# Performance work log

Measured on AMD Instinct MI355X. Metric: run time of the kernel, lower is better.

## Reference

```python
import jax, jax.numpy as jnp
import numpy as np

HIDDEN = 4096
N_HEADS = 32
NOPE = 128
ROPE = 64
Q_HEAD = NOPE + ROPE  # 192
V_HEAD = 128
KV_RANK = 512
EPS = 1e-6
THETA = 10000.0
SEQ = 2048


def setup_inputs() -> dict:
    key = jax.random.key(0)
    ks = jax.random.split(key, 6)
    s = lambda fi, fo: (2.0 / (fi + fo)) ** 0.5
    return {
        "positions": jnp.arange(SEQ, dtype=jnp.int64),
        "hidden_states": jax.random.normal(ks[0], (SEQ, HIDDEN), dtype=jnp.float32),
        "Wq": jax.random.normal(ks[1], (HIDDEN, N_HEADS * Q_HEAD), dtype=jnp.float32) * s(HIDDEN, N_HEADS * Q_HEAD),
        "Wkv_a": jax.random.normal(ks[2], (HIDDEN, KV_RANK + ROPE), dtype=jnp.float32) * s(HIDDEN, KV_RANK + ROPE),
        "ln_w": jnp.ones((KV_RANK,), dtype=jnp.float32),
        "Wkv_b": jax.random.normal(ks[3], (KV_RANK, N_HEADS * (NOPE + V_HEAD)), dtype=jnp.float32) * s(KV_RANK, N_HEADS * (NOPE + V_HEAD)),
        "Wo": jax.random.normal(ks[4], (N_HEADS * V_HEAD, HIDDEN), dtype=jnp.float32) * s(N_HEADS * V_HEAD, HIDDEN),
    }


def _rms_norm(x, w, eps=EPS):
    xf = x.astype(jnp.float32)
    var = jnp.mean(xf * xf, axis=-1, keepdims=True)
    return w * (xf * jax.lax.rsqrt(var + eps)).astype(x.dtype)


def _rope_cos_sin(positions):
    # neox-style rotary over ROPE dims
    inv_freq = 1.0 / (THETA ** (jnp.arange(0, ROPE, 2, dtype=jnp.float32) / ROPE))  # [ROPE/2]
    ang = positions.astype(jnp.float32)[:, None] * inv_freq[None, :]  # [S, ROPE/2]
    return jnp.cos(ang), jnp.sin(ang)


def _apply_rope(x, cos, sin):
    # x: [..., S, ROPE]; rotate-half (neox) convention
    x1, x2 = x[..., : ROPE // 2], x[..., ROPE // 2 :]
    return jnp.concatenate([x1 * cos - x2 * sin, x2 * cos + x1 * sin], axis=-1)


def reference(positions, hidden_states, Wq, Wkv_a, ln_w, Wkv_b, Wo):
    S = hidden_states.shape[0]
    scaling = Q_HEAD ** (-0.5)

    q = (hidden_states @ Wq).reshape(S, N_HEADS, Q_HEAD)
    q_pass, q_rot = q[..., :NOPE], q[..., NOPE:]

    ckv = hidden_states @ Wkv_a  # [S, KV_RANK + ROPE]
    k_lora, k_rot = ckv[:, :KV_RANK], ckv[:, KV_RANK:]

    kv = (_rms_norm(k_lora, ln_w) @ Wkv_b).reshape(S, N_HEADS, NOPE + V_HEAD)
    k_pass, v = kv[..., :NOPE], kv[..., NOPE:]

    cos, sin = _rope_cos_sin(positions)
    q_rot = _apply_rope(q_rot, cos[:, None, :], sin[:, None, :])  # [S,H,ROPE]
    k_rot = _apply_rope(k_rot, cos, sin)  # [S,ROPE], shared across heads

    qs = jnp.concatenate([q_pass, q_rot], axis=-1)  # [S,H,192]
    ks = jnp.concatenate([k_pass, jnp.broadcast_to(k_rot[:, None, :], (S, N_HEADS, ROPE))], axis=-1)

    # causal SDPA (value padded to q_head_dim then sliced back, as in source)
    scores = jnp.einsum("shd,thd->hst", qs, ks) * scaling  # [H,S,S]
    mask = jnp.tril(jnp.ones((S, S), dtype=bool))
    scores = jnp.where(mask[None], scores, jnp.finfo(scores.dtype).min)
    probs = jax.nn.softmax(scores, axis=-1)
    out = jnp.einsum("hst,thd->shd", probs, v)  # [S,H,V_HEAD]

    return out.reshape(S, N_HEADS * V_HEAD) @ Wo
```

## Files before the change

kernel.cpp:

```cpp
#include <hip/hip_runtime.h>


typedef __bf16 bf16x8 __attribute__((ext_vector_type(8)));
typedef float f32x4 __attribute__((ext_vector_type(4)));

#define SEQLEN 2048
#define NH 32
#define QH 192
#define QCN 6912
#define KVN 8192
#define HID 4096

#define AS1 __attribute__((address_space(1)))
#define AS3 __attribute__((address_space(3)))

__device__ __forceinline__ unsigned short f2b(float f) {
  union { float f; unsigned int u; } x; x.f = f;
  unsigned int r = (x.u + 0x7FFFu + ((x.u >> 16) & 1u)) >> 16;
  return (unsigned short)r;
}
__device__ __forceinline__ float b2f(unsigned short b) {
  union { unsigned int u; float f; } x; x.u = ((unsigned int)b) << 16;
  return x.f;
}

__global__ __launch_bounds__(256) void convk(const float* __restrict__ in,
                                             unsigned short* __restrict__ out,
                                             int n4) {
  int i = blockIdx.x * 256 + threadIdx.x;
  if (i < n4) {
    float4 v = ((const float4*)in)[i];
    ushort4 o;
    o.x = f2b(v.x); o.y = f2b(v.y); o.z = f2b(v.z); o.w = f2b(v.w);
    ((ushort4*)out)[i] = o;
  }
}

__global__ __launch_bounds__(256) void tconv(const float* __restrict__ in,
                                             unsigned short* __restrict__ out,
                                             int R, int Cin, int Cp) {
  __shared__ float t[64][65];
  const int r0 = blockIdx.x * 64, c0 = blockIdx.y * 64;
  const int tid = threadIdx.x;
#pragma unroll
  for (int i = 0; i < 16; ++i) {
    int idx = tid + i * 256;
    int rr = idx >> 6, cc = idx & 63;
    int c = c0 + cc;
    t[rr][cc] = (c < Cin) ? in[(size_t)(r0 + rr) * Cin + c] : 0.f;
  }
  __syncthreads();
#pragma unroll
  for (int i = 0; i < 16; ++i) {
    int idx = tid + i * 256;
    int cc = idx >> 6, rr = idx & 63;
    out[(size_t)(c0 + cc) * R + (r0 + rr)] = f2b(t[rr][cc]);
  }
}

template <int MH, int MHALF, int PAIR>
__device__ __forceinline__ void mmaq(f32x4 (*acc)[4], const bf16x8* aR, const bf16x8* bX) {
  __builtin_amdgcn_s_setprio(1);
#pragma unroll
  for (int i2 = 0; i2 < MH; ++i2)
#pragma unroll
    for (int kk = 0; kk < 2; ++kk)
#pragma unroll
      for (int j = 0; j < 2; ++j)
        acc[MHALF * MH + i2][PAIR * 2 + j] = __builtin_amdgcn_mfma_f32_16x16x32_bf16(
            aR[i2 * 2 + kk], bX[j * 2 + kk], acc[MHALF * MH + i2][PAIR * 2 + j], 0, 0, 0);
  __builtin_amdgcn_s_setprio(0);
}

#define PH_SYNC()                                        \
  __builtin_amdgcn_s_barrier();                          \
  asm volatile("s_waitcnt lgkmcnt(0)" ::: "memory");     \
  __builtin_amdgcn_sched_barrier(0)
#define PH_END() __builtin_amdgcn_s_barrier()

template <int BM, typename OutT>
__global__ __launch_bounds__(512, 2) void gemm8p(const unsigned short* __restrict__ A,
                                                 const unsigned short* __restrict__ B,
                                                 OutT* __restrict__ C,
                                                 int M, int N, int K) {
  constexpr int MF = BM / 32;
  constexpr int MH = MF / 2;
  constexpr int ARND = BM / 128;
  __shared__ __align__(16) unsigned short As[2][2][BM * 32];
  __shared__ __align__(16) unsigned short Bs[2][2][8192];

  const int tid = threadIdx.x;
  const int lane = tid & 63;
  const int w = tid >> 6;
  const int wr = w >> 2, wc = w & 3;
  const int l15 = lane & 15, lg = lane >> 4;
  const int ntn = N >> 8;
  const int bm = blockIdx.x / ntn, bn = blockIdx.x % ntn;
  const int m0 = bm * BM, n0 = bn << 8;

  auto stA = [&](int t, int h) {
    const int buf = t & 1, k0 = t << 6;
#pragma unroll
    for (int r = 0; r < ARND; ++r) {
      int u = r * 512 + tid;
      int blk = u >> 6, l = u & 63;
      int row = (blk >> 1) * 16 + (l & 15);
      int col = (blk & 1) * 32 + ((l >> 4) << 3);
      __builtin_amdgcn_global_load_lds(
          (const AS1 void*)(A + (size_t)(m0 + h * (BM / 2) + row) * K + (k0 + col)),
          (AS3 void*)(&As[buf][h][u * 8]), 16, 0, 0);
    }
  };
  auto stB = [&](int t, int h) {
    const int buf = t & 1, k0 = t << 6;
#pragma unroll
    for (int r = 0; r < 2; ++r) {
      int u = r * 512 + tid;
      int blk = u >> 6, l = u & 63;
      int row = (blk >> 1) * 16 + (l & 15);
      int col = (blk & 1) * 32 + ((l >> 4) << 3);
      __builtin_amdgcn_global_load_lds(
          (const AS1 void*)(B + (size_t)(n0 + h * 128 + row) * K + (k0 + col)),
          (AS3 void*)(&Bs[buf][h][u * 8]), 16, 0, 0);
    }
  };

  const f32x4 zero4 = {0.f, 0.f, 0.f, 0.f};
  f32x4 acc[MF][4];
#pragma unroll
  for (int i = 0; i < MF; ++i)
#pragma unroll
    for (int j = 0; j < 4; ++j) acc[i][j] = zero4;

  bf16x8 aR[MF], bA[4], bB[4];
  auto ldA = [&](int buf, int mhalf) {
#pragma unroll
    for (int i2 = 0; i2 < MH; ++i2)
#pragma unroll
      for (int kk = 0; kk < 2; ++kk)
        aR[i2 * 2 + kk] =
            *(const bf16x8*)&As[buf][wr][(((mhalf * MH + i2) * 2 + kk) * 64 + lane) * 8];
  };
  auto ldB = [&](int buf, int pair, bf16x8* dst) {
#pragma unroll
    for (int j = 0; j < 2; ++j)
#pragma unroll
      for (int kk = 0; kk < 2; ++kk)
        dst[j * 2 + kk] = *(const bf16x8*)
            &Bs[buf][wc >> 1][((((wc & 1) * 4 + pair * 2 + j) * 2 + kk) * 64 + lane) * 8];
  };

  const int nk = K >> 6;
  const int ni = nk >> 1;

  stA(0, 0); stA(0, 1); stB(0, 0); stB(0, 1);
  stB(1, 0); stB(1, 1);
  asm volatile("s_waitcnt vmcnt(4)" ::: "memory");
  __builtin_amdgcn_s_barrier();

#pragma unroll 1
  for (int i = 0; i < ni; ++i) {
    const int tO = 2 * i + 1, tN = 2 * i + 2, tN1 = 2 * i + 3;
    const bool pfN = tN < nk, pfN1 = tN1 < nk;
    const bool steady = (i + 1 < ni);
    ldA(0, 0); ldB(0, 0, bA); stA(tO, 0);
    PH_SYNC(); mmaq<MH, 0, 0>(acc, aR, bA); PH_END();
    ldB(0, 1, bB); stA(tO, 1);
    PH_SYNC(); mmaq<MH, 0, 1>(acc, aR, bB); PH_END();
    ldA(0, 1); if (pfN) stB(tN, 0);
    PH_SYNC(); mmaq<MH, 1, 1>(acc, aR, bB); PH_END();
    if (pfN) stB(tN, 1);
    if (steady) { asm volatile("s_waitcnt vmcnt(4)" ::: "memory"); }
    else        { asm volatile("s_waitcnt vmcnt(0)" ::: "memory"); }
    PH_SYNC(); mmaq<MH, 1, 0>(acc, aR, bA); PH_END();
    ldA(1, 0); ldB(1, 0, bA); if (pfN) stA(tN, 0);
    PH_SYNC(); mmaq<MH, 0, 0>(acc, aR, bA); PH_END();
    ldB(1, 1, bB); if (pfN) stA(tN, 1);
    PH_SYNC(); mmaq<MH, 0, 1>(acc, aR, bB); PH_END();
    ldA(1, 1); if (pfN1) stB(tN1, 0);
    PH_SYNC(); mmaq<MH, 1, 1>(acc, aR, bB); PH_END();
    if (pfN1) stB(tN1, 1);
    if (steady) { asm volatile("s_waitcnt vmcnt(4)" ::: "memory"); }
    else        { asm volatile("s_waitcnt vmcnt(0)" ::: "memory"); }
    PH_SYNC(); mmaq<MH, 1, 0>(acc, aR, bA); PH_END();
  }

  const int r0 = m0 + wr * (BM / 2), c0 = n0 + wc * 64;
#pragma unroll
  for (int mf = 0; mf < MF; ++mf)
#pragma unroll
    for (int nf = 0; nf < 4; ++nf) {
      int r = r0 + mf * 16 + lg * 4;
      int c = c0 + nf * 16 + l15;
#pragma unroll
      for (int i = 0; i < 4; ++i) {
        float v = acc[mf][nf][i];
        if constexpr (sizeof(OutT) == 2)
          ((unsigned short*)C)[(size_t)(r + i) * N + c] = f2b(v);
        else
          ((float*)C)[(size_t)(r + i) * N + c] = v;
      }
    }
}

__global__ __launch_bounds__(256) void rmsnorm_k(const unsigned short* __restrict__ qc,
                                                 const float* __restrict__ w,
                                                 unsigned short* __restrict__ out) {
  const int s = blockIdx.x;
  const int tid = threadIdx.x;
  const unsigned short* row = qc + (size_t)s * QCN + 6144;
  float x0 = b2f(row[tid]), x1 = b2f(row[tid + 256]);
  float ss = x0 * x0 + x1 * x1;
#pragma unroll
  for (int o = 1; o < 64; o <<= 1) ss += __shfl_xor(ss, o, 64);
  __shared__ float red[4];
  if ((tid & 63) == 0) red[tid >> 6] = ss;
  __syncthreads();
  float rs = rsqrtf((red[0] + red[1] + red[2] + red[3]) * (1.f / 512.f) + 1e-6f);
  out[(size_t)s * 512 + tid] = f2b(w[tid] * x0 * rs);
  out[(size_t)s * 512 + tid + 256] = f2b(w[tid + 256] * x1 * rs);
}

__global__ __launch_bounds__(256) void rope_q_k(unsigned short* __restrict__ qc) {
  int idx = blockIdx.x * 256 + threadIdx.x;
  int i = idx & 31, h = (idx >> 5) & 31, s = idx >> 10;
  float inv = exp2f(-(float)i * 0.4152410118609203f);
  float ang = (float)s * inv;
  float c = cosf(ang), sn = sinf(ang);
  size_t base = (size_t)s * QCN + h * QH + 128;
  float x1 = b2f(qc[base + i]), x2 = b2f(qc[base + 32 + i]);
  qc[base + i] = f2b(x1 * c - x2 * sn);
  qc[base + 32 + i] = f2b(x2 * c + x1 * sn);
}

__global__ __launch_bounds__(256) void rope_k_k(const unsigned short* __restrict__ qc,
                                                unsigned short* __restrict__ kr) {
  int idx = blockIdx.x * 256 + threadIdx.x;
  int i = idx & 31, s = idx >> 5;
  float inv = exp2f(-(float)i * 0.4152410118609203f);
  float ang = (float)s * inv;
  float c = cosf(ang), sn = sinf(ang);
  const unsigned short* row = qc + (size_t)s * QCN + 6144 + 512;
  float x1 = b2f(row[i]), x2 = b2f(row[32 + i]);
  kr[(size_t)s * 64 + i] = f2b(x1 * c - x2 * sn);
  kr[(size_t)s * 64 + 32 + i] = f2b(x2 * c + x1 * sn);
}

__global__ __launch_bounds__(256) void tv_k(const unsigned short* __restrict__ kv,
                                            unsigned short* __restrict__ vT) {
  __shared__ unsigned short t[64][66];
  const int t0 = blockIdx.x * 64, v0 = blockIdx.y * 64, h = blockIdx.z;
  const int tid = threadIdx.x;
#pragma unroll
  for (int i = 0; i < 16; ++i) {
    int idx = tid + i * 256;
    int rr = idx >> 6, cc = idx & 63;
    t[rr][cc] = kv[(size_t)(t0 + rr) * KVN + h * 256 + 128 + v0 + cc];
  }
  __syncthreads();
#pragma unroll
  for (int i = 0; i < 16; ++i) {
    int idx = tid + i * 256;
    int cc = idx >> 6, rr = idx & 63;
    vT[((size_t)h * 128 + v0 + cc) * SEQLEN + t0 + rr] = t[rr][cc];
  }
}

__global__ __launch_bounds__(256) void attn_k(const unsigned short* __restrict__ qc,
                                              const unsigned short* __restrict__ kv,
                                              const unsigned short* __restrict__ kr,
                                              const unsigned short* __restrict__ vT,
                                              unsigned short* __restrict__ ao) {
  __shared__ __align__(16) unsigned short Kt[64 * 192];
  __shared__ __align__(16) unsigned short Vt[128 * 72];
  __shared__ __align__(16) unsigned short Pl[4][32 * 72];

  const int tid = threadIdx.x;
  const int lane = tid & 63;
  const int w = tid >> 6;
  const int l15 = lane & 15, lg = lane >> 4;
  const int sw = l15 & 7;
  const int bid = blockIdx.x;
  const int qt = 15 - (bid >> 5);
  const int h = bid & 31;
  const int n_it = 2 * qt + 2;
  const int qrow_base = qt * 128 + w * 32;
  const float scale = 0.07216878364870323f;
  const f32x4 zero4 = {0.f, 0.f, 0.f, 0.f};

  bf16x8 kregs[4], rregs[2], vregs[4];

  auto loadregs = [&](int t0) {
#pragma unroll
    for (int p = 0; p < 4; ++p) {
      int id = tid + p * 256;
      kregs[p] = *(const bf16x8*)&kv[(size_t)(t0 + (id >> 4)) * KVN + h * 256 + (id & 15) * 8];
    }
#pragma unroll
    for (int p = 0; p < 2; ++p) {
      int id = tid + p * 256;
      rregs[p] = *(const bf16x8*)&kr[(size_t)(t0 + (id >> 3)) * 64 + (id & 7) * 8];
    }
#pragma unroll
    for (int p = 0; p < 4; ++p) {
      int id = tid + p * 256;
      vregs[p] = *(const bf16x8*)&vT[((size_t)h * 128 + (id >> 3)) * SEQLEN + t0 + (id & 7) * 8];
    }
  };
  auto writelds = [&]() {
#pragma unroll
    for (int p = 0; p < 4; ++p) {
      int id = tid + p * 256;
      int r = id >> 4, c16 = id & 15;
      *(bf16x8*)&Kt[r * 192 + ((c16 ^ (r & 7)) << 3)] = kregs[p];
    }
#pragma unroll
    for (int p = 0; p < 2; ++p) {
      int id = tid + p * 256;
      int r = id >> 3;
      *(bf16x8*)&Kt[r * 192 + ((16 + ((id & 7) ^ (r & 7))) << 3)] = rregs[p];
    }
#pragma unroll
    for (int p = 0; p < 4; ++p) {
      int id = tid + p * 256;
      *(bf16x8*)&Vt[(id >> 3) * 72 + (id & 7) * 8] = vregs[p];
    }
  };

  bf16x8 qf[2][6];
#pragma unroll
  for (int m = 0; m < 2; ++m) {
    const size_t qoff = (size_t)(qrow_base + m * 16 + l15) * QCN + (size_t)h * QH + lg * 8;
#pragma unroll
    for (int c = 0; c < 6; ++c) qf[m][c] = *(const bf16x8*)(qc + qoff + c * 32);
  }

  f32x4 o[2][8];
  float m_r[2], s_r[2];
#pragma unroll
  for (int m = 0; m < 2; ++m) {
#pragma unroll
    for (int vt = 0; vt < 8; ++vt) o[m][vt] = zero4;
    m_r[m] = -1e30f; s_r[m] = 0.f;
  }

  loadregs(0);

#pragma unroll 1
  for (int it = 0; it < n_it; ++it) {
    const int t0 = it * 64;
    writelds();
    __syncthreads();
    if (it + 1 < n_it) loadregs((it + 1) * 64);

    f32x4 st[2][4];
    __builtin_amdgcn_s_setprio(1);
#pragma unroll
    for (int tt = 0; tt < 4; ++tt) {
      f32x4 c0 = zero4, c1 = zero4;
      const int krow = (tt * 16 + l15) * 192;
#pragma unroll
      for (int c = 0; c < 6; ++c) {
        bf16x8 kf = *(const bf16x8*)&Kt[krow + (((c * 4 + lg) ^ sw) << 3)];
        c0 = __builtin_amdgcn_mfma_f32_16x16x32_bf16(kf, qf[0][c], c0, 0, 0, 0);
        c1 = __builtin_amdgcn_mfma_f32_16x16x32_bf16(kf, qf[1][c], c1, 0, 0, 0);
      }
      st[0][tt] = c0; st[1][tt] = c1;
    }
    __builtin_amdgcn_s_setprio(0);

    const bool domask = (t0 + 63 > qrow_base);
#pragma unroll
    for (int m = 0; m < 2; ++m) {
      const int qg = qrow_base + m * 16 + l15;
      float mx = -1e30f;
#pragma unroll
      for (int tt = 0; tt < 4; ++tt)
#pragma unroll
        for (int i = 0; i < 4; ++i) {
          float v = st[m][tt][i] * scale;
          if (domask) {
            int tg = t0 + tt * 16 + lg * 4 + i;
            v = (tg > qg) ? -1e30f : v;
          }
          st[m][tt][i] = v;
          mx = fmaxf(mx, v);
        }
      mx = fmaxf(mx, __shfl_xor(mx, 16, 64));
      mx = fmaxf(mx, __shfl_xor(mx, 32, 64));
      float mn = fmaxf(m_r[m], mx);
      float al = __expf(m_r[m] - mn);
      m_r[m] = mn;
      float ps = 0.f;
#pragma unroll
      for (int tt = 0; tt < 4; ++tt)
#pragma unroll
        for (int i = 0; i < 4; ++i) {
          float p = __expf(st[m][tt][i] - mn);
          st[m][tt][i] = p;
          ps += p;
        }
      ps += __shfl_xor(ps, 16, 64);
      ps += __shfl_xor(ps, 32, 64);
      s_r[m] = s_r[m] * al + ps;

#pragma unroll
      for (int tt = 0; tt < 4; ++tt) {
        ushort4 pk;
        pk.x = f2b(st[m][tt][0]); pk.y = f2b(st[m][tt][1]);
        pk.z = f2b(st[m][tt][2]); pk.w = f2b(st[m][tt][3]);
        *(ushort4*)&Pl[w][(m * 16 + l15) * 72 + tt * 16 + lg * 4] = pk;
      }
#pragma unroll
      for (int vt = 0; vt < 8; ++vt)
#pragma unroll
        for (int i = 0; i < 4; ++i) o[m][vt][i] *= al;
    }

    bf16x8 pa[2][2];
#pragma unroll
    for (int m = 0; m < 2; ++m)
#pragma unroll
      for (int ks = 0; ks < 2; ++ks)
        pa[m][ks] = *(const bf16x8*)&Pl[w][(m * 16 + l15) * 72 + ks * 32 + lg * 8];
    __builtin_amdgcn_s_setprio(1);
#pragma unroll
    for (int vt = 0; vt < 8; ++vt) {
      bf16x8 b0 = *(const bf16x8*)&Vt[(vt * 16 + l15) * 72 + lg * 8];
      bf16x8 b1 = *(const bf16x8*)&Vt[(vt * 16 + l15) * 72 + 32 + lg * 8];
#pragma unroll
      for (int m = 0; m < 2; ++m) {
        o[m][vt] = __builtin_amdgcn_mfma_f32_16x16x32_bf16(b0, pa[m][0], o[m][vt], 0, 0, 0);
        o[m][vt] = __builtin_amdgcn_mfma_f32_16x16x32_bf16(b1, pa[m][1], o[m][vt], 0, 0, 0);
      }
    }
    __builtin_amdgcn_s_setprio(0);
    __syncthreads();
  }

#pragma unroll
  for (int m = 0; m < 2; ++m) {
    float rs = 1.f / s_r[m];
    int qg = qrow_base + m * 16 + l15;
#pragma unroll
    for (int vt = 0; vt < 8; ++vt) {
      ushort4 pk;
      pk.x = f2b(o[m][vt][0] * rs); pk.y = f2b(o[m][vt][1] * rs);
      pk.z = f2b(o[m][vt][2] * rs); pk.w = f2b(o[m][vt][3] * rs);
      *(ushort4*)&ao[(size_t)qg * (NH * 128) + h * 128 + vt * 16 + lg * 4] = pk;
    }
  }
}

extern "C" void kernel_launch(void* const* d_in, const int* in_sizes, int n_in,
                              void* d_out, int out_size, void* d_ws, size_t ws_size,
                              hipStream_t stream) {
  (void)in_sizes; (void)n_in; (void)out_size; (void)ws_size;
  const float* hs = (const float*)d_in[1];
  const float* Wq = (const float*)d_in[2];
  const float* Wkva = (const float*)d_in[3];
  const float* lnw = (const float*)d_in[4];
  const float* Wkvb = (const float*)d_in[5];
  const float* Wo = (const float*)d_in[6];
  float* out = (float*)d_out;
  char* ws = (char*)d_ws;

  constexpr size_t OFF_HSBF = 0;
  constexpr size_t OFF_WQT = OFF_HSBF + (size_t)2048 * 4096 * 2;
  constexpr size_t OFF_WKVAT = OFF_WQT + (size_t)6144 * 4096 * 2;
  constexpr size_t OFF_WKVBT = OFF_WKVAT + (size_t)640 * 4096 * 2;
  constexpr size_t OFF_WOT = OFF_WKVBT + (size_t)8192 * 512 * 2;
  constexpr size_t OFF_QC = OFF_WOT + (size_t)4096 * 4096 * 2;
  constexpr size_t OFF_CKVN = OFF_QC + (size_t)2048 * 6912 * 2;
  constexpr size_t OFF_KR = OFF_CKVN + (size_t)2048 * 512 * 2;
  constexpr size_t OFF_KV = OFF_KR + (size_t)2048 * 64 * 2;
  constexpr size_t OFF_VT = OFF_KV + (size_t)2048 * 8192 * 2;
  constexpr size_t OFF_AO = OFF_VT + (size_t)32 * 128 * 2048 * 2;

  unsigned short* hs_bf = (unsigned short*)(ws + OFF_HSBF);
  unsigned short* WqT = (unsigned short*)(ws + OFF_WQT);
  unsigned short* WkvaT = (unsigned short*)(ws + OFF_WKVAT);
  unsigned short* WkvbT = (unsigned short*)(ws + OFF_WKVBT);
  unsigned short* WoT = (unsigned short*)(ws + OFF_WOT);
  unsigned short* qcbuf = (unsigned short*)(ws + OFF_QC);
  unsigned short* ckvn = (unsigned short*)(ws + OFF_CKVN);
  unsigned short* kr = (unsigned short*)(ws + OFF_KR);
  unsigned short* kvbuf = (unsigned short*)(ws + OFF_KV);
  unsigned short* vT = (unsigned short*)(ws + OFF_VT);
  unsigned short* ao = (unsigned short*)(ws + OFF_AO);

  convk<<<dim3(8192), 256, 0, stream>>>(hs, hs_bf, 2048 * 4096 / 4);
  tconv<<<dim3(64, 96), 256, 0, stream>>>(Wq, WqT, 4096, 6144, 6144);
  tconv<<<dim3(64, 10), 256, 0, stream>>>(Wkva, WkvaT, 4096, 576, 640);
  tconv<<<dim3(8, 128), 256, 0, stream>>>(Wkvb, WkvbT, 512, 8192, 8192);
  tconv<<<dim3(64, 64), 256, 0, stream>>>(Wo, WoT, 4096, 4096, 4096);

  gemm8p<256, unsigned short><<<dim3(8 * 27), 512, 0, stream>>>(hs_bf, WqT, qcbuf, 2048, QCN, 4096);
  rmsnorm_k<<<dim3(2048), 256, 0, stream>>>(qcbuf, lnw, ckvn);
  rope_k_k<<<dim3(256), 256, 0, stream>>>(qcbuf, kr);
  gemm8p<256, unsigned short><<<dim3(8 * 32), 512, 0, stream>>>(ckvn, WkvbT, kvbuf, 2048, 8192, 512);
  rope_q_k<<<dim3(8192), 256, 0, stream>>>(qcbuf);
  tv_k<<<dim3(32, 2, 32), 256, 0, stream>>>(kvbuf, vT);
  attn_k<<<dim3(512), 256, 0, stream>>>(qcbuf, kvbuf, kr, vT, ao);
  gemm8p<128, float><<<dim3(16 * 16), 512, 0, stream>>>(ao, WoT, out, 2048, 4096, 4096);
}
```

Baseline: 523.8 us.

## Fold softmax scale into Wq, lazy rescale, packed bf16 convert, swizzle GEMM blocks

The attention scale is moved into the Wq transpose-convert pass, so scores no longer need a per-element multiply. The online softmax now skips updating the running max and rescaling the output accumulators unless the new block max exceeds the old one by more than 8 across the whole wavefront. P is converted to bf16 with the packed v_cvt_pk_bf16_f32 instruction instead of manual rounding. The GEMM block index is remapped into groups of 8 M-tiles for better L2 reuse. The lazy rescale lets probabilities grow up to e^8 before rescaling, which slightly changes numerical behaviour.

```diff
diff --git a/kernel.cpp b/kernel.cpp
--- a/kernel.cpp
+++ b/kernel.cpp
@@ -38,7 +38,7 @@
 
 __global__ __launch_bounds__(256) void tconv(const float* __restrict__ in,
                                              unsigned short* __restrict__ out,
-                                             int R, int Cin, int Cp) {
+                                             int R, int Cin, int Cp, float scl) {
   __shared__ float t[64][65];
   const int r0 = blockIdx.x * 64, c0 = blockIdx.y * 64;
   const int tid = threadIdx.x;
@@ -47,7 +47,7 @@
     int idx = tid + i * 256;
     int rr = idx >> 6, cc = idx & 63;
     int c = c0 + cc;
-    t[rr][cc] = (c < Cin) ? in[(size_t)(r0 + rr) * Cin + c] : 0.f;
+    t[rr][cc] = (c < Cin) ? in[(size_t)(r0 + rr) * Cin + c] * scl : 0.f;
   }
   __syncthreads();
 #pragma unroll
@@ -95,7 +95,9 @@
   const int wr = w >> 2, wc = w & 3;
   const int l15 = lane & 15, lg = lane >> 4;
   const int ntn = N >> 8;
-  const int bm = blockIdx.x / ntn, bn = blockIdx.x % ntn;
+  const int g = blockIdx.x & 7, s = blockIdx.x >> 3;
+  const int bn = s % ntn;
+  const int bm = g + 8 * (s / ntn);
   const int m0 = bm * BM, n0 = bn << 8;
 
   auto stA = [&](int t, int h) {
@@ -285,7 +287,6 @@
   const int h = bid & 31;
   const int n_it = 2 * qt + 2;
   const int qrow_base = qt * 128 + w * 32;
-  const float scale = 0.07216878364870323f;
   const f32x4 zero4 = {0.f, 0.f, 0.f, 0.f};
 
   bf16x8 kregs[4], rregs[2], vregs[4];
@@ -378,7 +379,7 @@
       for (int tt = 0; tt < 4; ++tt)
 #pragma unroll
         for (int i = 0; i < 4; ++i) {
-          float v = st[m][tt][i] * scale;
+          float v = st[m][tt][i];
           if (domask) {
             int tg = t0 + tt * 16 + lg * 4 + i;
             v = (tg > qg) ? -1e30f : v;
@@ -388,9 +389,19 @@
         }
       mx = fmaxf(mx, __shfl_xor(mx, 16, 64));
       mx = fmaxf(mx, __shfl_xor(mx, 32, 64));
-      float mn = fmaxf(m_r[m], mx);
-      float al = __expf(m_r[m] - mn);
-      m_r[m] = mn;
+      float mn;
+      if (__all(mx - m_r[m] <= 8.f)) {
+        mn = m_r[m];
+      } else {
+        mn = fmaxf(m_r[m], mx);
+        float al = __expf(m_r[m] - mn);
+        m_r[m] = mn;
+        s_r[m] *= al;
+#pragma unroll
+        for (int vt = 0; vt < 8; ++vt)
+#pragma unroll
+          for (int i = 0; i < 4; ++i) o[m][vt][i] *= al;
+      }
       float ps = 0.f;
 #pragma unroll
       for (int tt = 0; tt < 4; ++tt)
@@ -402,19 +413,16 @@
         }
       ps += __shfl_xor(ps, 16, 64);
       ps += __shfl_xor(ps, 32, 64);
-      s_r[m] = s_r[m] * al + ps;
+      s_r[m] += ps;
 
 #pragma unroll
       for (int tt = 0; tt < 4; ++tt) {
-        ushort4 pk;
-        pk.x = f2b(st[m][tt][0]); pk.y = f2b(st[m][tt][1]);
-        pk.z = f2b(st[m][tt][2]); pk.w = f2b(st[m][tt][3]);
-        *(ushort4*)&Pl[w][(m * 16 + l15) * 72 + tt * 16 + lg * 4] = pk;
+        unsigned int r0, r1;
+        asm("v_cvt_pk_bf16_f32 %0, %1, %2" : "=v"(r0) : "v"(st[m][tt][0]), "v"(st[m][tt][1]));
+        asm("v_cvt_pk_bf16_f32 %0, %1, %2" : "=v"(r1) : "v"(st[m][tt][2]), "v"(st[m][tt][3]));
+        uint2 pk; pk.x = r0; pk.y = r1;
+        *(uint2*)&Pl[w][(m * 16 + l15) * 72 + tt * 16 + lg * 4] = pk;
       }
-#pragma unroll
-      for (int vt = 0; vt < 8; ++vt)
-#pragma unroll
-        for (int i = 0; i < 4; ++i) o[m][vt][i] *= al;
     }
 
     bf16x8 pa[2][2];
@@ -490,10 +498,10 @@
   unsigned short* ao = (unsigned short*)(ws + OFF_AO);
 
   convk<<<dim3(8192), 256, 0, stream>>>(hs, hs_bf, 2048 * 4096 / 4);
-  tconv<<<dim3(64, 96), 256, 0, stream>>>(Wq, WqT, 4096, 6144, 6144);
-  tconv<<<dim3(64, 10), 256, 0, stream>>>(Wkva, WkvaT, 4096, 576, 640);
-  tconv<<<dim3(8, 128), 256, 0, stream>>>(Wkvb, WkvbT, 512, 8192, 8192);
-  tconv<<<dim3(64, 64), 256, 0, stream>>>(Wo, WoT, 4096, 4096, 4096);
+  tconv<<<dim3(64, 96), 256, 0, stream>>>(Wq, WqT, 4096, 6144, 6144, 0.07216878364870323f);
+  tconv<<<dim3(64, 10), 256, 0, stream>>>(Wkva, WkvaT, 4096, 576, 640, 1.f);
+  tconv<<<dim3(8, 128), 256, 0, stream>>>(Wkvb, WkvbT, 512, 8192, 8192, 1.f);
+  tconv<<<dim3(64, 64), 256, 0, stream>>>(Wo, WoT, 4096, 4096, 4096, 1.f);
 
   gemm8p<256, unsigned short><<<dim3(8 * 27), 512, 0, stream>>>(hs_bf, WqT, qcbuf, 2048, QCN, 4096);
   rmsnorm_k<<<dim3(2048), 256, 0, stream>>>(qcbuf, lnw, ckvn);
```

Measured after the change: 520.0 us. About the same (-0.7%).
